# Optimization experiments

Hardware: AMD Instinct MI355X
Metric: run time of the kernel (lower is better)

Reference implementation:

```python
import jax, jax.numpy as jnp
import numpy as np

N = 100000
E = 1600000
IN_C, HID_C, OUT_C = 128, 64, 64
LAYERS = 2


def setup_inputs() -> dict:
    key = jax.random.key(0)
    ks = jax.random.split(key, 7)
    x = jax.random.normal(ks[0], (N, IN_C), dtype=jnp.float32)
    edge_index = jax.random.randint(ks[1], (2, E), 0, N, dtype=jnp.int32)
    W_init = jax.random.normal(ks[2], (IN_C, HID_C), dtype=jnp.float32) / np.sqrt(IN_C)
    W_self = jax.random.normal(ks[3], (LAYERS, HID_C, HID_C), dtype=jnp.float32) / np.sqrt(HID_C)
    W_agg = jax.random.normal(ks[4], (LAYERS, HID_C, HID_C), dtype=jnp.float32) / np.sqrt(HID_C)
    b = jnp.zeros((LAYERS, HID_C), dtype=jnp.float32)
    W_out = jax.random.normal(ks[5], (HID_C, OUT_C), dtype=jnp.float32) / np.sqrt(HID_C)
    return {"x": x, "edge_index": edge_index, "W_init": W_init,
            "W_self": W_self, "W_agg": W_agg, "b": b, "W_out": W_out}


def reference(x, edge_index, W_init, W_self, W_agg, b, W_out):
    # edge (dst, src): aggregated_neighbors[edge[0]].append(x[edge[1]])
    dst = edge_index[0]
    src = edge_index[1]
    n = x.shape[0]
    # in-degree for mean aggregation (clamp to 1 for isolated nodes)
    deg = jax.ops.segment_sum(jnp.ones((src.shape[0],), dtype=x.dtype), dst,
                              num_segments=n)
    deg = jnp.maximum(deg, 1.0)[:, None]  # [N,1]
    h = x @ W_init  # initialize: [N, hid]
    for l in range(LAYERS):
        msgs = h[src]  # per-edge gather [E, hid]
        agg = jax.ops.segment_sum(msgs, dst, num_segments=n) / deg  # mean aggregate
        h = jax.nn.relu(agg @ W_agg[l] + h @ W_self[l] + b[l])  # combine
    return h @ W_out  # output: [N, out]
```

## Files before the change

kernel.cpp:

```cpp
#include <hip/hip_runtime.h>
#include <hip/hip_fp16.h>

#define N_NODES 100000
#define E_EDGES 1600000
#define IN_C    128
#define HID_C   64
#define OUT_C   64
#define ROWS    32
#define NBUCK   391
#define BSHIFT  8
#define BNODES  256
#define CAP     5120
#define CHUNK   4096
#define NB_BINCH 391
#define NB_TR   112
#define IDXCAP  1632
#define IDXMAX  1568

typedef _Float16 f16x8 __attribute__((ext_vector_type(8)));
typedef float    f32x4 __attribute__((ext_vector_type(4)));
#define MFMA16(a, b, c) __builtin_amdgcn_mfma_f32_16x16x32_f16(a, b, c, 0, 0, 0)

struct BinS {
    int hist[NBUCK]; int resbase[NBUCK]; int cur[NBUCK];
    unsigned pk[CHUNK]; unsigned short bk[CHUNK];
};

__global__ __launch_bounds__(256) void k1_bin_tr(const int* __restrict__ ei,
                                                 int* __restrict__ bucket_cursor,
                                                 unsigned* __restrict__ gbuck,
                                                 const float* __restrict__ Wi,
                                                 const float* __restrict__ Wsf,
                                                 const float* __restrict__ Waf,
                                                 const float* __restrict__ Wo,
                                                 _Float16* __restrict__ wtr) {
    __shared__ BinS S;
    int tid = threadIdx.x;
    if (blockIdx.x < NB_BINCH) {
        for (int i = tid; i < NBUCK; i += 256) S.hist[i] = 0;
        __syncthreads();
        int base = blockIdx.x * CHUNK;
        for (int i = tid; i < CHUNK; i += 256) {
            int e = base + i;
            if (e < E_EDGES) {
                int dst = ei[e];
                int src = ei[E_EDGES + e];
                int b = dst >> BSHIFT;
                S.pk[i] = ((unsigned)(dst & (BNODES - 1)) << 17) | (unsigned)src;
                S.bk[i] = (unsigned short)b;
                atomicAdd(&S.hist[b], 1);
            } else S.bk[i] = 0xFFFF;
        }
        __syncthreads();
        for (int i = tid; i < NBUCK; i += 256) {
            S.resbase[i] = atomicAdd(&bucket_cursor[i], S.hist[i]);
            S.cur[i] = 0;
        }
        __syncthreads();
        for (int i = tid; i < CHUNK; i += 256) {
            if (S.bk[i] != 0xFFFF) {
                int b = S.bk[i];
                int slot = S.resbase[b] + atomicAdd(&S.cur[b], 1);
                if (slot < CAP) gbuck[(size_t)b * CAP + slot] = S.pk[i];
            }
        }
    } else {
        int t = (blockIdx.x - NB_BINCH) * 256 + tid;
        if (t < 8192) {
            int k = t >> 6, col = t & 63;
            wtr[col * 136 + k] = (_Float16)Wi[t];
        } else if (t < 24576) {
            int u = t - 8192; int l = u >> 13; int v = u & 8191;
            int k = v >> 6, col = v & 63;
            float w = (k < 64) ? Waf[l * 4096 + k * 64 + col] : Wsf[l * 4096 + (k - 64) * 64 + col];
            wtr[8704 + l * 8704 + col * 136 + k] = (_Float16)w;
        } else if (t < 28672) {
            int u = t - 24576; int k = u >> 6, col = u & 63;
            wtr[26112 + col * 72 + k] = (_Float16)Wo[u];
        }
    }
}

struct InitS { _Float16 sA[ROWS][IN_C + 8]; _Float16 sBt[HID_C][IN_C + 8]; };
struct BuildS { int lcnt[BNODES]; int lpos[BNODES]; int lcur[BNODES]; int s[2][512]; };
union K2S { InitS ini; BuildS bld; };

template<int K>
__device__ __forceinline__ void mfma_tile(const _Float16* sA, const _Float16* sBt,
                                          int lane, int wave, f32x4 acc[2]) {
    const int LDA = K + 8;
    int r0 = (wave >> 1) * 16;
    int wc = wave & 1;
    int m = lane & 15, kg = lane >> 4;
    acc[0] = (f32x4){0.f, 0.f, 0.f, 0.f};
    acc[1] = (f32x4){0.f, 0.f, 0.f, 0.f};
    #pragma unroll
    for (int ks = 0; ks < K / 32; ++ks) {
        f16x8 a = *(const f16x8*)&sA[(r0 + m) * LDA + 32 * ks + 8 * kg];
        #pragma unroll
        for (int nt = 0; nt < 2; ++nt) {
            f16x8 b = *(const f16x8*)&sBt[(wc * 32 + nt * 16 + m) * LDA + 32 * ks + 8 * kg];
            acc[nt] = MFMA16(a, b, acc[nt]);
        }
    }
}

__global__ __launch_bounds__(256) void k2_build_init(const unsigned* __restrict__ gbuck,
                                                     const int* __restrict__ bucket_cursor,
                                                     int* __restrict__ csr,
                                                     int2* __restrict__ rc,
                                                     const float* __restrict__ x,
                                                     const float4* __restrict__ wtrI,
                                                     __half* __restrict__ h) {
    __shared__ K2S U;
    int t = threadIdx.x;
    if (blockIdx.x < NBUCK) {
        BuildS& S = U.bld;
        int b = blockIdx.x;
        int v0 = (t < NBUCK) ? min(bucket_cursor[t], CAP) : 0;
        int v1 = (t + 256 < NBUCK) ? min(bucket_cursor[t + 256], CAP) : 0;
        S.s[0][t] = v0; S.s[0][t + 256] = v1;
        S.lcnt[t] = 0; S.lcur[t] = 0;
        __syncthreads();
        int p = 0;
        for (int off = 1; off < 512; off <<= 1) {
            int a0 = S.s[p][t]       + ((t >= off)       ? S.s[p][t - off] : 0);
            int a1 = S.s[p][t + 256] + ((t + 256 >= off) ? S.s[p][t + 256 - off] : 0);
            S.s[p ^ 1][t] = a0; S.s[p ^ 1][t + 256] = a1;
            __syncthreads();
            p ^= 1;
        }
        int bb = (b == 0) ? 0 : S.s[p][b - 1];
        int ec = min(bucket_cursor[b], CAP);
        int gnode = b * BNODES;
        int nn = min(BNODES, N_NODES - gnode);
        const unsigned* mybuck = gbuck + (size_t)b * CAP;
        __syncthreads();
        for (int i = t; i < ec; i += 256) atomicAdd(&S.lcnt[mybuck[i] >> 17], 1);
        __syncthreads();
        int c = S.lcnt[t];
        S.s[0][t] = c;
        __syncthreads();
        int q = 0;
        for (int off = 1; off < 256; off <<= 1) {
            int a0 = S.s[q][t] + ((t >= off) ? S.s[q][t - off] : 0);
            S.s[q ^ 1][t] = a0;
            __syncthreads();
            q ^= 1;
        }
        int ex = S.s[q][t] - c;
        S.lpos[t] = ex;
        if (t < nn) rc[gnode + t] = make_int2(bb + ex, c);
        __syncthreads();
        for (int i = t; i < ec; i += 256) {
            unsigned pkt = mybuck[i];
            int dl = pkt >> 17;
            int slot = S.lpos[dl] + atomicAdd(&S.lcur[dl], 1);
            csr[bb + slot] = (int)(pkt & 0x1FFFF);
        }
    } else {
        InitS& S = U.ini;
        int row0 = (blockIdx.x - NBUCK) * ROWS;
        float4* sB4 = (float4*)&S.sBt[0][0];
        for (int i = t; i < 1088; i += 256) sB4[i] = wtrI[i];
        const float4* x4 = (const float4*)x;
        for (int i = t; i < ROWS * 32; i += 256) {
            int r = i >> 5, qq = i & 31;
            float4 f = x4[(size_t)(row0 + r) * 32 + qq];
            __half2 ha = __floats2half2_rn(f.x, f.y), hb = __floats2half2_rn(f.z, f.w);
            uint2 u; u.x = *(unsigned*)&ha; u.y = *(unsigned*)&hb;
            *(uint2*)&S.sA[r][qq * 4] = u;
        }
        __syncthreads();
        int lane = t & 63, wave = t >> 6;
        f32x4 acc[2];
        mfma_tile<IN_C>(&S.sA[0][0], &S.sBt[0][0], lane, wave, acc);
        int m = lane & 15, rg = lane >> 4;
        int r0 = (wave >> 1) * 16, wc = wave & 1;
        #pragma unroll
        for (int nt = 0; nt < 2; ++nt) {
            int col = wc * 32 + nt * 16 + m;
            #pragma unroll
            for (int i = 0; i < 4; ++i) {
                int row = row0 + r0 + rg * 4 + i;
                h[(size_t)row * HID_C + col] = __float2half(acc[nt][i]);
            }
        }
    }
}

#define GCHUNK(r, JB, CLAMP)                                                    \
    {                                                                           \
        _Pragma("unroll")                                                       \
        for (int s = 0; s < 4; ++s) {                                           \
            int ee = (JB) + s * 4 + g4;                                         \
            int a = sl[r] + ee;                                                 \
            if (CLAMP) a = min(a, IDXCAP - 1);                                  \
            int src = sIdx[a];                                                  \
            uint2 vv = h2u[(size_t)src * 16 + c16];                             \
            bool ok = ee < dd[r];                                               \
            unsigned vx = ok ? vv.x : 0u, vy = ok ? vv.y : 0u;                  \
            p01[r] += *(__half2*)&vx;                                           \
            p23[r] += *(__half2*)&vy;                                           \
        }                                                                       \
    }

template<bool FINAL>
__global__ __launch_bounds__(256) void fused_layer(const __half* __restrict__ h,
                                                   const int2* __restrict__ rc,
                                                   const int* __restrict__ csr,
                                                   const float4* __restrict__ wtrL,
                                                   const float* __restrict__ bias,
                                                   __half* __restrict__ hout,
                                                   const float4* __restrict__ wtrO,
                                                   float* __restrict__ out) {
    __shared__ _Float16 sA[ROWS][136];
    __shared__ _Float16 sBt[HID_C][136];
    __shared__ int sIdx[IDXCAP];
    __shared__ int2 sRC[ROWS];
    int tid = threadIdx.x;
    float4* sB4 = (float4*)&sBt[0][0];
    for (int i = tid; i < 1088; i += 256) sB4[i] = wtrL[i];
    int row0 = blockIdx.x * ROWS;
    const uint2* h2u = (const uint2*)h;

    if (tid < 32) sRC[tid] = rc[row0 + tid];
    int2 rcF = rc[row0];
    int2 rcL = rc[row0 + 31];
    int e0 = __builtin_amdgcn_readfirstlane(rcF.x);
    int e1 = __builtin_amdgcn_readfirstlane(rcL.x) + __builtin_amdgcn_readfirstlane(rcL.y);
    int Lc = min(e1 - e0, IDXMAX);
    for (int i = tid; i < Lc; i += 256) sIdx[i] = csr[e0 + i];
    if (tid < 64) sIdx[min(Lc + tid, IDXCAP - 1)] = 0;
    for (int i = tid; i < 512; i += 256) {
        int r = i >> 4, qq = i & 15;
        *(uint2*)&sA[r][64 + qq * 4] = h2u[(size_t)(row0 + r) * 16 + qq];
    }
    __syncthreads();

    int wave = tid >> 6, lane = tid & 63;
    int g4 = lane >> 4;
    int c16 = lane & 15;
    int sl[8], dd[8];
    #pragma unroll
    for (int r = 0; r < 8; ++r) {
        int2 v = sRC[wave * 8 + r];
        sl[r] = min(__builtin_amdgcn_readfirstlane(v.x) - e0, IDXMAX);
        dd[r] = __builtin_amdgcn_readfirstlane(v.y);
    }
    const __half2 hzero = __floats2half2_rn(0.f, 0.f);
    __half2 p01[8], p23[8];
    #pragma unroll
    for (int r = 0; r < 8; ++r) { p01[r] = hzero; p23[r] = hzero; }

    #pragma unroll
    for (int r = 0; r < 8; ++r) GCHUNK(r, 0, false)
    #pragma unroll
    for (int r = 0; r < 8; ++r) GCHUNK(r, 16, false)
    int dmax = dd[0];
    #pragma unroll
    for (int r = 1; r < 8; ++r) dmax = max(dmax, dd[r]);
    if (dmax > 32) {
        #pragma unroll
        for (int r = 0; r < 8; ++r)
            for (int j = 32; j < dd[r]; j += 16) GCHUNK(r, j, true)
    }

    #pragma unroll
    for (int r = 0; r < 8; ++r) {
        unsigned u01 = *(unsigned*)&p01[r], u23 = *(unsigned*)&p23[r];
        unsigned o01 = (unsigned)__shfl_xor((int)u01, 16);
        unsigned o23 = (unsigned)__shfl_xor((int)u23, 16);
        p01[r] += *(__half2*)&o01; p23[r] += *(__half2*)&o23;
        u01 = *(unsigned*)&p01[r]; u23 = *(unsigned*)&p23[r];
        o01 = (unsigned)__shfl_xor((int)u01, 32);
        o23 = (unsigned)__shfl_xor((int)u23, 32);
        p01[r] += *(__half2*)&o01; p23[r] += *(__half2*)&o23;
        if (lane < 16) {
            __half2 hinv = __float2half2_rn(1.f / fmaxf((float)dd[r], 1.f));
            __half2 q01 = p01[r] * hinv, q23 = p23[r] * hinv;
            uint2 agg2; agg2.x = *(unsigned*)&q01; agg2.y = *(unsigned*)&q23;
            *(uint2*)&sA[wave * 8 + r][4 * c16] = agg2;
        }
    }
    __syncthreads();

    f32x4 acc[2];
    mfma_tile<128>(&sA[0][0], &sBt[0][0], lane, wave, acc);
    int m = lane & 15, rg = lane >> 4;
    int r0 = (wave >> 1) * 16, wc = wave & 1;
    if (!FINAL) {
        #pragma unroll
        for (int nt = 0; nt < 2; ++nt) {
            int col = wc * 32 + nt * 16 + m;
            float bv = bias[col];
            #pragma unroll
            for (int i = 0; i < 4; ++i) {
                int row = row0 + r0 + rg * 4 + i;
                hout[(size_t)row * HID_C + col] = __float2half(fmaxf(acc[nt][i] + bv, 0.f));
            }
        }
    } else {
        __syncthreads();
        _Float16* sA72 = &sA[0][0];
        #pragma unroll
        for (int nt = 0; nt < 2; ++nt) {
            int col = wc * 32 + nt * 16 + m;
            float bv = bias[col];
            #pragma unroll
            for (int i = 0; i < 4; ++i) {
                int rl = r0 + rg * 4 + i;
                sA72[rl * 72 + col] = (_Float16)fmaxf(acc[nt][i] + bv, 0.f);
            }
        }
        for (int i = tid; i < 576; i += 256) sB4[i] = wtrO[i];
        __syncthreads();
        f32x4 acc2[2];
        mfma_tile<64>(&sA[0][0], &sBt[0][0], lane, wave, acc2);
        #pragma unroll
        for (int nt = 0; nt < 2; ++nt) {
            int col = wc * 32 + nt * 16 + m;
            #pragma unroll
            for (int i = 0; i < 4; ++i) {
                int row = row0 + r0 + rg * 4 + i;
                out[(size_t)row * OUT_C + col] = acc2[nt][i];
            }
        }
    }
}

extern "C" void kernel_launch(void* const* d_in, const int* in_sizes, int n_in,
                              void* d_out, int out_size, void* d_ws, size_t ws_size,
                              hipStream_t stream) {
    const float* x      = (const float*)d_in[0];
    const int*   ei     = (const int*)  d_in[1];
    const float* W_init = (const float*)d_in[2];
    const float* W_self = (const float*)d_in[3];
    const float* W_agg  = (const float*)d_in[4];
    const float* b      = (const float*)d_in[5];
    const float* W_out  = (const float*)d_in[6];
    float* out = (float*)d_out;

    char* ws = (char*)d_ws;
    const size_t KB = 1 << 10;
    int*      bucket_cursor = (int*)(ws + 0);
    int2*     rc            = (int2*)(ws + 4 * KB);
    int*      csr           = (int*)(ws + 1024 * KB);
    _Float16* wtr           = (_Float16*)(ws + 7424 * KB);
    unsigned* gbuck         = (unsigned*)(ws + 8192 * KB);
    __half*   hA            = (__half*)(ws + 18432 * KB);
    __half*   hB            = (__half*)(ws + 32768 * KB);

    const float4* wtrI  = (const float4*)(wtr);
    const float4* wtrL0 = (const float4*)(wtr + 8704);
    const float4* wtrL1 = (const float4*)(wtr + 17408);
    const float4* wtrO  = (const float4*)(wtr + 26112);

    hipMemsetAsync(bucket_cursor, 0, NBUCK * sizeof(int), stream);
    k1_bin_tr<<<NB_BINCH + NB_TR, 256, 0, stream>>>(ei, bucket_cursor, gbuck,
                                                    W_init, W_self, W_agg, W_out, wtr);
    k2_build_init<<<NBUCK + N_NODES / ROWS, 256, 0, stream>>>(gbuck, bucket_cursor, csr, rc,
                                                              x, wtrI, hA);
    const int GB = N_NODES / ROWS;
    fused_layer<false><<<GB, 256, 0, stream>>>(hA, rc, csr, wtrL0, b + 0 * HID_C, hB,
                                               wtrO, out);
    fused_layer<true><<<GB, 256, 0, stream>>>(hB, rc, csr, wtrL1, b + 1 * HID_C, hA,
                                              wtrO, out);
}
```

Baseline: 144.0 us.

## Hold layer weights in registers and use dynamic 8-edge gather loop

Each wave now loads its slice of the layer weight matrix (and of the output weights in the final layer) straight from global memory into registers, instead of staging the whole matrix in shared memory. This frees about 17 KB of LDS per block, and a launch-bounds hint asks for 5 blocks per CU. The fixed 32-edge unrolled gather plus a clamped tail loop is replaced by a loop over chunks of 8 edges up to the largest degree in the wave, which skips chunks for rows whose degree is already covered. Keeping the weights in registers raises VGPR pressure, and the dynamic loop gives less memory-level parallelism per row.

```diff
diff --git a/kernel.cpp b/kernel.cpp
--- a/kernel.cpp
+++ b/kernel.cpp
@@ -102,6 +102,18 @@
             f16x8 b = *(const f16x8*)&sBt[(wc * 32 + nt * 16 + m) * LDA + 32 * ks + 8 * kg];
             acc[nt] = MFMA16(a, b, acc[nt]);
         }
+    }
+}
+
+template<int NKS>
+__device__ __forceinline__ void mfma_regB(const _Float16* aBase, int lda, int m,
+                                          int kg, const f16x8* bf0, const f16x8* bf1,
+                                          f32x4 acc[2]) {
+    #pragma unroll
+    for (int ks = 0; ks < NKS; ++ks) {
+        f16x8 a = *(const f16x8*)&aBase[m * lda + 32 * ks + 8 * kg];
+        acc[0] = MFMA16(a, bf0[ks], acc[0]);
+        acc[1] = MFMA16(a, bf1[ks], acc[1]);
     }
 }
 
@@ -189,40 +201,30 @@
     }
 }
 
-#define GCHUNK(r, JB, CLAMP)                                                    \
-    {                                                                           \
-        _Pragma("unroll")                                                       \
-        for (int s = 0; s < 4; ++s) {                                           \
-            int ee = (JB) + s * 4 + g4;                                         \
-            int a = sl[r] + ee;                                                 \
-            if (CLAMP) a = min(a, IDXCAP - 1);                                  \
-            int src = sIdx[a];                                                  \
-            uint2 vv = h2u[(size_t)src * 16 + c16];                             \
-            bool ok = ee < dd[r];                                               \
-            unsigned vx = ok ? vv.x : 0u, vy = ok ? vv.y : 0u;                  \
-            p01[r] += *(__half2*)&vx;                                           \
-            p23[r] += *(__half2*)&vy;                                           \
-        }                                                                       \
-    }
-
 template<bool FINAL>
-__global__ __launch_bounds__(256) void fused_layer(const __half* __restrict__ h,
-                                                   const int2* __restrict__ rc,
-                                                   const int* __restrict__ csr,
-                                                   const float4* __restrict__ wtrL,
-                                                   const float* __restrict__ bias,
-                                                   __half* __restrict__ hout,
-                                                   const float4* __restrict__ wtrO,
-                                                   float* __restrict__ out) {
+__global__ __launch_bounds__(256, 5) void fused_layer(const __half* __restrict__ h,
+                                                      const int2* __restrict__ rc,
+                                                      const int* __restrict__ csr,
+                                                      const _Float16* __restrict__ wB,
+                                                      const float* __restrict__ bias,
+                                                      __half* __restrict__ hout,
+                                                      const _Float16* __restrict__ wO,
+                                                      float* __restrict__ out) {
     __shared__ _Float16 sA[ROWS][136];
-    __shared__ _Float16 sBt[HID_C][136];
     __shared__ int sIdx[IDXCAP];
     __shared__ int2 sRC[ROWS];
     int tid = threadIdx.x;
-    float4* sB4 = (float4*)&sBt[0][0];
-    for (int i = tid; i < 1088; i += 256) sB4[i] = wtrL[i];
+    int wave = tid >> 6, lane = tid & 63;
+    int m = lane & 15, kg = lane >> 4, wc = wave & 1;
     int row0 = blockIdx.x * ROWS;
     const uint2* h2u = (const uint2*)h;
+
+    f16x8 bf0[4], bf1[4];
+    #pragma unroll
+    for (int ks = 0; ks < 4; ++ks) {
+        bf0[ks] = *(const f16x8*)&wB[(wc * 32 + m) * 136 + 32 * ks + 8 * kg];
+        bf1[ks] = *(const f16x8*)&wB[(wc * 32 + 16 + m) * 136 + 32 * ks + 8 * kg];
+    }
 
     if (tid < 32) sRC[tid] = rc[row0 + tid];
     int2 rcF = rc[row0];
@@ -238,32 +240,38 @@
     }
     __syncthreads();
 
-    int wave = tid >> 6, lane = tid & 63;
     int g4 = lane >> 4;
     int c16 = lane & 15;
     int sl[8], dd[8];
+    int dmax = 0;
     #pragma unroll
     for (int r = 0; r < 8; ++r) {
         int2 v = sRC[wave * 8 + r];
         sl[r] = min(__builtin_amdgcn_readfirstlane(v.x) - e0, IDXMAX);
         dd[r] = __builtin_amdgcn_readfirstlane(v.y);
+        dmax = max(dmax, dd[r]);
     }
     const __half2 hzero = __floats2half2_rn(0.f, 0.f);
     __half2 p01[8], p23[8];
     #pragma unroll
     for (int r = 0; r < 8; ++r) { p01[r] = hzero; p23[r] = hzero; }
 
-    #pragma unroll
-    for (int r = 0; r < 8; ++r) GCHUNK(r, 0, false)
-    #pragma unroll
-    for (int r = 0; r < 8; ++r) GCHUNK(r, 16, false)
-    int dmax = dd[0];
-    #pragma unroll
-    for (int r = 1; r < 8; ++r) dmax = max(dmax, dd[r]);
-    if (dmax > 32) {
-        #pragma unroll
-        for (int r = 0; r < 8; ++r)
-            for (int j = 32; j < dd[r]; j += 16) GCHUNK(r, j, true)
+    for (int c8 = 0; c8 < dmax; c8 += 8) {
+        #pragma unroll
+        for (int r = 0; r < 8; ++r) {
+            if (c8 < dd[r]) {
+                #pragma unroll
+                for (int s = 0; s < 2; ++s) {
+                    int ee = c8 + s * 4 + g4;
+                    int src = sIdx[sl[r] + ee];
+                    uint2 vv = h2u[(size_t)src * 16 + c16];
+                    bool ok = ee < dd[r];
+                    unsigned vx = ok ? vv.x : 0u, vy = ok ? vv.y : 0u;
+                    p01[r] += *(__half2*)&vx;
+                    p23[r] += *(__half2*)&vy;
+                }
+            }
+        }
     }
 
     #pragma unroll
@@ -286,18 +294,21 @@
     __syncthreads();
 
     f32x4 acc[2];
-    mfma_tile<128>(&sA[0][0], &sBt[0][0], lane, wave, acc);
-    int m = lane & 15, rg = lane >> 4;
-    int r0 = (wave >> 1) * 16, wc = wave & 1;
+    acc[0] = (f32x4){0.f, 0.f, 0.f, 0.f};
+    acc[1] = (f32x4){0.f, 0.f, 0.f, 0.f};
+    int r0 = (wave >> 1) * 16;
+    mfma_regB<4>(&sA[r0][0], 136, m, kg, bf0, bf1, acc);
+    int rg = lane >> 4;
     if (!FINAL) {
         #pragma unroll
         for (int nt = 0; nt < 2; ++nt) {
             int col = wc * 32 + nt * 16 + m;
             float bv = bias[col];
+            f32x4 a = (nt == 0) ? acc[0] : acc[1];
             #pragma unroll
             for (int i = 0; i < 4; ++i) {
                 int row = row0 + r0 + rg * 4 + i;
-                hout[(size_t)row * HID_C + col] = __float2half(fmaxf(acc[nt][i] + bv, 0.f));
+                hout[(size_t)row * HID_C + col] = __float2half(fmaxf(a[i] + bv, 0.f));
             }
         }
     } else {
@@ -307,23 +318,32 @@
         for (int nt = 0; nt < 2; ++nt) {
             int col = wc * 32 + nt * 16 + m;
             float bv = bias[col];
+            f32x4 a = (nt == 0) ? acc[0] : acc[1];
             #pragma unroll
             for (int i = 0; i < 4; ++i) {
                 int rl = r0 + rg * 4 + i;
-                sA72[rl * 72 + col] = (_Float16)fmaxf(acc[nt][i] + bv, 0.f);
-            }
-        }
-        for (int i = tid; i < 576; i += 256) sB4[i] = wtrO[i];
+                sA72[rl * 72 + col] = (_Float16)fmaxf(a[i] + bv, 0.f);
+            }
+        }
+        f16x8 of0[2], of1[2];
+        #pragma unroll
+        for (int ks = 0; ks < 2; ++ks) {
+            of0[ks] = *(const f16x8*)&wO[(wc * 32 + m) * 72 + 32 * ks + 8 * kg];
+            of1[ks] = *(const f16x8*)&wO[(wc * 32 + 16 + m) * 72 + 32 * ks + 8 * kg];
+        }
         __syncthreads();
         f32x4 acc2[2];
-        mfma_tile<64>(&sA[0][0], &sBt[0][0], lane, wave, acc2);
+        acc2[0] = (f32x4){0.f, 0.f, 0.f, 0.f};
+        acc2[1] = (f32x4){0.f, 0.f, 0.f, 0.f};
+        mfma_regB<2>(&sA72[r0 * 72], 72, m, kg, of0, of1, acc2);
         #pragma unroll
         for (int nt = 0; nt < 2; ++nt) {
             int col = wc * 32 + nt * 16 + m;
+            f32x4 a = (nt == 0) ? acc2[0] : acc2[1];
             #pragma unroll
             for (int i = 0; i < 4; ++i) {
                 int row = row0 + r0 + rg * 4 + i;
-                out[(size_t)row * OUT_C + col] = acc2[nt][i];
+                out[(size_t)row * OUT_C + col] = a[i];
             }
         }
     }
@@ -351,10 +371,10 @@
     __half*   hA            = (__half*)(ws + 18432 * KB);
     __half*   hB            = (__half*)(ws + 32768 * KB);
 
-    const float4* wtrI  = (const float4*)(wtr);
-    const float4* wtrL0 = (const float4*)(wtr + 8704);
-    const float4* wtrL1 = (const float4*)(wtr + 17408);
-    const float4* wtrO  = (const float4*)(wtr + 26112);
+    const float4*   wtrI  = (const float4*)(wtr);
+    const _Float16* wtrL0 = wtr + 8704;
+    const _Float16* wtrL1 = wtr + 17408;
+    const _Float16* wtrO  = wtr + 26112;
 
     hipMemsetAsync(bucket_cursor, 0, NBUCK * sizeof(int), stream);
     k1_bin_tr<<<NB_BINCH + NB_TR, 256, 0, stream>>>(ei, bucket_cursor, gbuck,
```

After: 136.9 us. 1.05x faster.
